# Kernel optimization log

Hardware: AMD Instinct MI355X
Metric: run time of the kernel (lower is better)

## Reference

```python
import jax, jax.numpy as jnp
import numpy as np

T, B, E, H = 2048, 2, 1024, 16
DH = E // H  # head_dim = 64


def setup_inputs() -> dict:
    key = jax.random.key(0)
    ks = jax.random.split(key, 5)
    query = jax.random.normal(ks[0], (T, B, E), dtype=jnp.float32)
    # self-attention: key/value are passed but unused by the module
    k_in = query
    v_in = query
    # xavier-ish scaled params
    in_proj_weight = jax.random.normal(ks[1], (3 * E, E), dtype=jnp.float32) * (E ** -0.5)
    in_proj_bias = jnp.zeros((3 * E,), dtype=jnp.float32)
    out_w = jax.random.normal(ks[2], (E, E), dtype=jnp.float32) * (E ** -0.5)
    out_b = jnp.zeros((E,), dtype=jnp.float32)
    return {"query": query, "key": k_in, "value": v_in,
            "in_proj_weight": in_proj_weight, "in_proj_bias": in_proj_bias,
            "out_w": out_w, "out_b": out_b}


def reference(query, key, value, in_proj_weight, in_proj_bias, out_w, out_b):
    # query: [T, B, E] (fairseq Time x Batch x Channel)
    t, b, e = query.shape
    scaling = DH ** -0.5
    # fused QKV projection: in_proj_weight [3E, E]
    qkv = jnp.einsum('tbe,fe->tbf', query, in_proj_weight) + in_proj_bias  # [T,B,3E]
    q, k, v = jnp.split(qkv, 3, axis=-1)
    q = q * scaling
    # split heads -> [T, B, H, DH]
    q = q.reshape(t, b, H, DH)
    k = k.reshape(t, b, H, DH)
    v = v.reshape(t, b, H, DH)
    # attention scores [B, H, T, T]
    scores = jnp.einsum('tbhd,sbhd->bhts', q, k)
    probs = jax.nn.softmax(scores, axis=-1)
    # weighted sum -> [T, B, H, DH] -> [T, B, E]
    attn = jnp.einsum('bhts,sbhd->tbhd', probs, v).reshape(t, b, e)
    # output projection (LinearSuper with sample dims == super dims)
    out = jnp.einsum('tbe,oe->tbo', attn, out_w) + out_b
    return out
```

## Files before the change

### kernel.cpp

```cpp
#include <hip/hip_runtime.h>
#include <hip/hip_bf16.h>
#include <stdint.h>
#include <math.h>

#define T_DIM 2048
#define B_DIM 2
#define E_DIM 1024
#define H_DIM 16
#define DH    64
#define MROWS (T_DIM * B_DIM)
#define QKVN  (3 * E_DIM)

typedef __attribute__((ext_vector_type(8))) __bf16 bf16x8;
typedef __attribute__((ext_vector_type(4))) float f32x4;
typedef __attribute__((ext_vector_type(4))) uint32_t u32x4;
typedef __attribute__((ext_vector_type(2))) uint32_t u32x2;

typedef __attribute__((address_space(1))) const uint32_t gu32;
typedef __attribute__((address_space(3))) uint32_t lu32;

#define GLL(gp, lp) __builtin_amdgcn_global_load_lds((gu32*)(gp), (lu32*)(lp), 16, 0, 0)

#define QSCALE 0.18033688011112042f

#if __has_builtin(__builtin_amdgcn_exp2f)
#define EXP2(x) __builtin_amdgcn_exp2f(x)
#else
#define EXP2(x) exp2f(x)
#endif

static __device__ __forceinline__ unsigned short f2bf(float f) {
    uint32_t u = __float_as_uint(f);
    u += 0x7FFFu + ((u >> 16) & 1u);
    return (unsigned short)(u >> 16);
}

__global__ void k_cvt3(const float* __restrict__ q,  const float* __restrict__ w,
                       const float* __restrict__ o,
                       unsigned short* __restrict__ qo, unsigned short* __restrict__ wo,
                       unsigned short* __restrict__ oo) {
    long i = (long)(blockIdx.x * 256 + threadIdx.x) * 8;
    const float* src; unsigned short* dst; long off;
    if (i < 4194304)      { src = q; dst = qo; off = i; }
    else if (i < 7340032) { src = w; dst = wo; off = i - 4194304; }
    else                  { src = o; dst = oo; off = i - 7340032; }
    float4 a = *(const float4*)(src + off);
    float4 b = *(const float4*)(src + off + 4);
    union { unsigned short s[8]; u32x4 v; } r;
    r.s[0] = f2bf(a.x); r.s[1] = f2bf(a.y); r.s[2] = f2bf(a.z); r.s[3] = f2bf(a.w);
    r.s[4] = f2bf(b.x); r.s[5] = f2bf(b.y); r.s[6] = f2bf(b.z); r.s[7] = f2bf(b.w);
    *(u32x4*)(dst + off) = r.v;
}

template <int STORE_BF16, int SCALE_Q>
__global__ __launch_bounds__(256) void k_gemm_bt(
    const unsigned short* __restrict__ A,
    const unsigned short* __restrict__ B,
    const float* __restrict__ bias,
    void* __restrict__ C,
    int M, int N, int K)
{
    __shared__ unsigned short As[128 * 64];
    __shared__ unsigned short Bs[128 * 64];
    const int tid = threadIdx.x;
    const int wid = tid >> 6, lane = tid & 63;
    const int m0 = blockIdx.y * 128, n0 = blockIdx.x * 128;

    const unsigned short* ag[4];
    const unsigned short* bg[4];
    unsigned lo[4];
#pragma unroll
    for (int j = 0; j < 4; ++j) {
        int o = (wid * 4 + j) * 1024 + lane * 16;
        int r = o >> 7;
        int c = (o >> 4) & 7;
        int cs = (c ^ (r & 7)) * 8;
        ag[j] = A + (long)(m0 + r) * K + cs;
        bg[j] = B + (long)(n0 + r) * K + cs;
        lo[j] = (unsigned)((wid * 4 + j) * 1024);
    }

    f32x4 acc[4][4] = {};
    const int wr = wid >> 1, wc = wid & 1;
    const int nk = K >> 6;

    for (int kt = 0; kt < nk; ++kt) {
#pragma unroll
        for (int j = 0; j < 4; ++j) {
            GLL(ag[j], (char*)As + lo[j]);
            GLL(bg[j], (char*)Bs + lo[j]);
            ag[j] += 64;
            bg[j] += 64;
        }
        __syncthreads();

        bf16x8 af[4][2], bfr[4][2];
#pragma unroll
        for (int i = 0; i < 4; ++i) {
            int ra = wr * 64 + i * 16 + (lane & 15);
            int rb = wc * 64 + i * 16 + (lane & 15);
#pragma unroll
            for (int kk = 0; kk < 2; ++kk) {
                int sa = ((kk * 4 + (lane >> 4)) ^ (ra & 7)) * 16;
                int sb = ((kk * 4 + (lane >> 4)) ^ (rb & 7)) * 16;
                af[i][kk]  = *(const bf16x8*)((char*)As + ra * 128 + sa);
                bfr[i][kk] = *(const bf16x8*)((char*)Bs + rb * 128 + sb);
            }
        }
#pragma unroll
        for (int kk = 0; kk < 2; ++kk)
#pragma unroll
            for (int mi = 0; mi < 4; ++mi)
#pragma unroll
                for (int ni = 0; ni < 4; ++ni)
                    acc[mi][ni] = __builtin_amdgcn_mfma_f32_16x16x32_bf16(
                        af[mi][kk], bfr[ni][kk], acc[mi][ni], 0, 0, 0);
        __syncthreads();
    }

#pragma unroll
    for (int mi = 0; mi < 4; ++mi)
#pragma unroll
        for (int ni = 0; ni < 4; ++ni) {
            int col = n0 + wc * 64 + ni * 16 + (lane & 15);
            float bv = bias[col];
            float scl = (SCALE_Q && col < 1024) ? QSCALE : 1.0f;
#pragma unroll
            for (int r = 0; r < 4; ++r) {
                int row = m0 + wr * 64 + mi * 16 + (lane >> 4) * 4 + r;
                float v = (acc[mi][ni][r] + bv) * scl;
                if (STORE_BF16)
                    ((unsigned short*)C)[(long)row * N + col] = f2bf(v);
                else
                    ((float*)C)[(long)row * N + col] = v;
            }
        }
}

__global__ __launch_bounds__(256) void k_transpose_v(
    const unsigned short* __restrict__ qkv, unsigned short* __restrict__ Vt)
{
    __shared__ unsigned short tile[64 * 64];
    const int bh = blockIdx.x >> 5, tt = blockIdx.x & 31;
    const int b = bh >> 4, h = bh & 15;
    const int tid = threadIdx.x;

    {
        int tr = tid >> 3;
        int s0 = tid & 7;
#pragma unroll
        for (int rr = 0; rr < 2; ++rr) {
            int t = tr + rr * 32;
            u32x4 v = *(const u32x4*)(qkv + ((long)(tt * 64 + t) * 2 + b) * 3072 + 2048 + h * 64 + s0 * 8);
            int slot = s0 ^ (t & 7) ^ ((t >> 3) & 7);
            *(u32x4*)((char*)tile + t * 128 + slot * 16) = v;
        }
    }
    __syncthreads();
    {
        int d = tid >> 3;
        int t8 = (tid & 7) * 8;
#pragma unroll
        for (int rr = 0; rr < 2; ++rr) {
            int dd = d + rr * 32;
            union { unsigned short s[8]; u32x4 v; } r;
#pragma unroll
            for (int i = 0; i < 8; ++i) {
                int pos = t8 + i;
                int t = (pos >> 2) + 16 * (pos & 3);
                int slot = (dd >> 3) ^ (t & 7) ^ ((t >> 3) & 7);
                r.s[i] = *(const unsigned short*)((char*)tile + t * 128 + slot * 16 + (dd & 7) * 2);
            }
            *(u32x4*)(Vt + ((long)bh * 64 + dd) * 2048 + tt * 64 + t8) = r.v;
        }
    }
}

__global__ __launch_bounds__(256, 2) void k_attn(
    const unsigned short* __restrict__ qkv,
    const unsigned short* __restrict__ Vt,
    unsigned short* __restrict__ attn)
{
    __shared__ unsigned short Ks[2 * 64 * 64];
    __shared__ unsigned short Vs[2 * 64 * 64];
    __shared__ unsigned short Ps[4 * 32 * 64];
    const int tid = threadIdx.x, wid = tid >> 6, lane = tid & 63;
    const int bh = blockIdx.x >> 4, tq = blockIdx.x & 15;
    const int b = bh >> 4, h = bh & 15;

    bf16x8 qf[2][2];
#pragma unroll
    for (int mi = 0; mi < 2; ++mi)
#pragma unroll
        for (int kk = 0; kk < 2; ++kk) {
            int t = tq * 128 + wid * 32 + mi * 16 + (lane & 15);
            qf[mi][kk] = *(const bf16x8*)(qkv + (long)(t * 2 + b) * 3072 + h * 64 + kk * 32 + (lane >> 4) * 8);
        }

    const unsigned short* kg[2];
    const unsigned short* vg[2];
    unsigned lo[2];
#pragma unroll
    for (int j = 0; j < 2; ++j) {
        int o = (wid * 2 + j) * 1024 + lane * 16;
        int r = o >> 7, c = (o >> 4) & 7;
        int cs = (c ^ (r & 7)) * 8;
        kg[j] = qkv + (long)(r * 2 + b) * 3072 + 1024 + h * 64 + cs;
        vg[j] = Vt + ((long)bh * 64 + r) * 2048 + cs;
        lo[j] = (unsigned)((wid * 2 + j) * 1024);
    }

    union { uint32_t u[4]; bf16x8 v; } onesu;
    onesu.u[0] = onesu.u[1] = onesu.u[2] = onesu.u[3] = 0x3F803F80u;
    const bf16x8 ones = onesu.v;

    f32x4 acc[2][4] = {};
    f32x4 suma[2] = {};

#pragma unroll
    for (int j = 0; j < 2; ++j) {
        GLL(kg[j], (char*)Ks + lo[j]);
        GLL(vg[j], (char*)Vs + lo[j]);
        kg[j] += 64 * 6144;
        vg[j] += 64;
    }

    for (int st = 0; st < 32; ++st) {
        const int cur = st & 1;
        if (st < 31) {
#pragma unroll
            for (int j = 0; j < 2; ++j) {
                GLL(kg[j], (char*)Ks + (cur ^ 1) * 8192 + lo[j]);
                GLL(vg[j], (char*)Vs + (cur ^ 1) * 8192 + lo[j]);
                kg[j] += 64 * 6144;
                vg[j] += 64;
            }
            asm volatile("s_waitcnt vmcnt(4)" ::: "memory");
        } else {
            asm volatile("s_waitcnt vmcnt(0)" ::: "memory");
        }
        __builtin_amdgcn_s_barrier();

        const char* kbase = (const char*)Ks + cur * 8192;
        const char* vbase = (const char*)Vs + cur * 8192;

        bf16x8 kf[4][2];
#pragma unroll
        for (int ni = 0; ni < 4; ++ni) {
            int row = ni * 16 + (lane & 15);
#pragma unroll
            for (int kk = 0; kk < 2; ++kk) {
                int sl = ((kk * 4 + (lane >> 4)) ^ (row & 7)) * 16;
                kf[ni][kk] = *(const bf16x8*)(kbase + row * 128 + sl);
            }
        }
        f32x4 sc[2][4] = {};
#pragma unroll
        for (int kk = 0; kk < 2; ++kk)
#pragma unroll
            for (int mi = 0; mi < 2; ++mi)
#pragma unroll
                for (int ni = 0; ni < 4; ++ni)
                    sc[mi][ni] = __builtin_amdgcn_mfma_f32_16x16x32_bf16(
                        qf[mi][kk], kf[ni][kk], sc[mi][ni], 0, 0, 0);

        const int c = lane & 15;
#pragma unroll
        for (int mi = 0; mi < 2; ++mi)
#pragma unroll
            for (int r = 0; r < 4; ++r) {
                float e0 = EXP2(sc[mi][0][r]);
                float e1 = EXP2(sc[mi][1][r]);
                float e2 = EXP2(sc[mi][2][r]);
                float e3 = EXP2(sc[mi][3][r]);
                int q = mi * 16 + (lane >> 4) * 4 + r;
                u32x2 w;
                w.x = (uint32_t)f2bf(e0) | ((uint32_t)f2bf(e1) << 16);
                w.y = (uint32_t)f2bf(e2) | ((uint32_t)f2bf(e3) << 16);
                int off = wid * 4096 + q * 128 + (((c >> 1) ^ (q & 7)) << 4) + (c & 1) * 8;
                *(u32x2*)((char*)Ps + off) = w;
            }

        bf16x8 pf[2][2], vf[4][2];
#pragma unroll
        for (int mi = 0; mi < 2; ++mi)
#pragma unroll
            for (int kk = 0; kk < 2; ++kk) {
                int q = mi * 16 + (lane & 15);
                int sl = ((kk * 4 + (lane >> 4)) ^ (q & 7)) * 16;
                pf[mi][kk] = *(const bf16x8*)((char*)Ps + wid * 4096 + q * 128 + sl);
            }
#pragma unroll
        for (int nd = 0; nd < 4; ++nd) {
            int row = nd * 16 + (lane & 15);
#pragma unroll
            for (int kk = 0; kk < 2; ++kk) {
                int sl = ((kk * 4 + (lane >> 4)) ^ (row & 7)) * 16;
                vf[nd][kk] = *(const bf16x8*)(vbase + row * 128 + sl);
            }
        }
#pragma unroll
        for (int kk = 0; kk < 2; ++kk)
#pragma unroll
            for (int mi = 0; mi < 2; ++mi) {
                suma[mi] = __builtin_amdgcn_mfma_f32_16x16x32_bf16(
                    pf[mi][kk], ones, suma[mi], 0, 0, 0);
#pragma unroll
                for (int nd = 0; nd < 4; ++nd)
                    acc[mi][nd] = __builtin_amdgcn_mfma_f32_16x16x32_bf16(
                        pf[mi][kk], vf[nd][kk], acc[mi][nd], 0, 0, 0);
            }
        __builtin_amdgcn_s_barrier();
    }

#pragma unroll
    for (int mi = 0; mi < 2; ++mi)
#pragma unroll
        for (int nd = 0; nd < 4; ++nd)
#pragma unroll
            for (int r = 0; r < 4; ++r) {
                int t = tq * 128 + wid * 32 + mi * 16 + (lane >> 4) * 4 + r;
                int e = h * 64 + nd * 16 + (lane & 15);
                attn[(long)(t * 2 + b) * 1024 + e] = f2bf(acc[mi][nd][r] / suma[mi][r]);
            }
}

extern "C" void kernel_launch(void* const* d_in, const int* in_sizes, int n_in,
                              void* d_out, int out_size, void* d_ws, size_t ws_size,
                              hipStream_t stream) {
    const float* query = (const float*)d_in[0];
    const float* ipw   = (const float*)d_in[3];
    const float* ipb   = (const float*)d_in[4];
    const float* ow    = (const float*)d_in[5];
    const float* ob    = (const float*)d_in[6];
    float* out = (float*)d_out;

    char* ws = (char*)d_ws;
    unsigned short* Xb   = (unsigned short*)(ws);
    unsigned short* Wb   = (unsigned short*)(ws + (8l << 20));
    unsigned short* OWb  = (unsigned short*)(ws + (14l << 20));
    unsigned short* qkvp = (unsigned short*)(ws + (16l << 20));
    unsigned short* Vtp  = (unsigned short*)(ws + (40l << 20));
    unsigned short* attn = (unsigned short*)(ws + (48l << 20));

    k_cvt3<<<4096, 256, 0, stream>>>(query, ipw, ow, Xb, Wb, OWb);

    k_gemm_bt<1, 1><<<dim3(QKVN / 128, MROWS / 128), 256, 0, stream>>>(
        Xb, Wb, ipb, qkvp, MROWS, QKVN, E_DIM);

    k_transpose_v<<<1024, 256, 0, stream>>>(qkvp, Vtp);

    k_attn<<<512, 256, 0, stream>>>(qkvp, Vtp, attn);

    k_gemm_bt<0, 0><<<dim3(E_DIM / 128, MROWS / 128), 256, 0, stream>>>(
        attn, OWb, ob, out, MROWS, E_DIM, E_DIM);
}
```

Measured before the change: 225.4 us.

## Software-pipeline attention loop so QK^T overlaps previous step's PV

```diff
diff --git a/kernel.cpp b/kernel.cpp
--- a/kernel.cpp
+++ b/kernel.cpp
@@ -183,7 +183,7 @@
 {
     __shared__ unsigned short Ks[2 * 64 * 64];
     __shared__ unsigned short Vs[2 * 64 * 64];
-    __shared__ unsigned short Ps[4 * 32 * 64];
+    __shared__ unsigned short Ps[2 * 4 * 32 * 64];
     const int tid = threadIdx.x, wid = tid >> 6, lane = tid & 63;
     const int bh = blockIdx.x >> 4, tq = blockIdx.x & 15;
     const int b = bh >> 4, h = bh & 15;
@@ -216,34 +216,26 @@
 
     f32x4 acc[2][4] = {};
     f32x4 suma[2] = {};
+    bf16x8 vf[4][2];
+
+    const int c = lane & 15;
 
 #pragma unroll
     for (int j = 0; j < 2; ++j) {
         GLL(kg[j], (char*)Ks + lo[j]);
         GLL(vg[j], (char*)Vs + lo[j]);
-        kg[j] += 64 * 6144;
-        vg[j] += 64;
-    }
-
-    for (int st = 0; st < 32; ++st) {
-        const int cur = st & 1;
-        if (st < 31) {
-#pragma unroll
-            for (int j = 0; j < 2; ++j) {
-                GLL(kg[j], (char*)Ks + (cur ^ 1) * 8192 + lo[j]);
-                GLL(vg[j], (char*)Vs + (cur ^ 1) * 8192 + lo[j]);
-                kg[j] += 64 * 6144;
-                vg[j] += 64;
-            }
-            asm volatile("s_waitcnt vmcnt(4)" ::: "memory");
-        } else {
-            asm volatile("s_waitcnt vmcnt(0)" ::: "memory");
-        }
-        __builtin_amdgcn_s_barrier();
-
-        const char* kbase = (const char*)Ks + cur * 8192;
-        const char* vbase = (const char*)Vs + cur * 8192;
-
+        kg[j] += 64 * 6144;  vg[j] += 64;
+    }
+#pragma unroll
+    for (int j = 0; j < 2; ++j) {
+        GLL(kg[j], (char*)Ks + 8192 + lo[j]);
+        GLL(vg[j], (char*)Vs + 8192 + lo[j]);
+        kg[j] += 64 * 6144;  vg[j] += 64;
+    }
+    asm volatile("s_waitcnt vmcnt(4)" ::: "memory");
+    __builtin_amdgcn_s_barrier();
+
+    {
         bf16x8 kf[4][2];
 #pragma unroll
         for (int ni = 0; ni < 4; ++ni) {
@@ -251,7 +243,7 @@
 #pragma unroll
             for (int kk = 0; kk < 2; ++kk) {
                 int sl = ((kk * 4 + (lane >> 4)) ^ (row & 7)) * 16;
-                kf[ni][kk] = *(const bf16x8*)(kbase + row * 128 + sl);
+                kf[ni][kk] = *(const bf16x8*)((char*)Ks + row * 128 + sl);
             }
         }
         f32x4 sc[2][4] = {};
@@ -263,8 +255,6 @@
                 for (int ni = 0; ni < 4; ++ni)
                     sc[mi][ni] = __builtin_amdgcn_mfma_f32_16x16x32_bf16(
                         qf[mi][kk], kf[ni][kk], sc[mi][ni], 0, 0, 0);
-
-        const int c = lane & 15;
 #pragma unroll
         for (int mi = 0; mi < 2; ++mi)
 #pragma unroll
@@ -280,25 +270,69 @@
                 int off = wid * 4096 + q * 128 + (((c >> 1) ^ (q & 7)) << 4) + (c & 1) * 8;
                 *(u32x2*)((char*)Ps + off) = w;
             }
-
-        bf16x8 pf[2][2], vf[4][2];
+#pragma unroll
+        for (int nd = 0; nd < 4; ++nd) {
+            int row = nd * 16 + (lane & 15);
+#pragma unroll
+            for (int kk = 0; kk < 2; ++kk) {
+                int sl = ((kk * 4 + (lane >> 4)) ^ (row & 7)) * 16;
+                vf[nd][kk] = *(const bf16x8*)((char*)Vs + row * 128 + sl);
+            }
+        }
+    }
+
+    for (int st = 1; st < 32; ++st) {
+        const int cur = st & 1;
+        asm volatile("s_waitcnt lgkmcnt(0)" ::: "memory");
+        __builtin_amdgcn_s_barrier();
+        __builtin_amdgcn_sched_barrier(0);
+        if (st < 31) {
+#pragma unroll
+            for (int j = 0; j < 2; ++j) {
+                GLL(kg[j], (char*)Ks + (cur ^ 1) * 8192 + lo[j]);
+                GLL(vg[j], (char*)Vs + (cur ^ 1) * 8192 + lo[j]);
+                kg[j] += 64 * 6144;  vg[j] += 64;
+            }
+            asm volatile("s_waitcnt vmcnt(4)" ::: "memory");
+        } else {
+            asm volatile("s_waitcnt vmcnt(0)" ::: "memory");
+        }
+        __builtin_amdgcn_s_barrier();
+
+        const char* kbase = (const char*)Ks + cur * 8192;
+        const char* vbase = (const char*)Vs + cur * 8192;
+        char* pw = (char*)Ps + cur * 16384 + wid * 4096;
+        const char* pr = (const char*)Ps + (cur ^ 1) * 16384 + wid * 4096;
+
+        bf16x8 kf[4][2];
+#pragma unroll
+        for (int ni = 0; ni < 4; ++ni) {
+            int row = ni * 16 + (lane & 15);
+#pragma unroll
+            for (int kk = 0; kk < 2; ++kk) {
+                int sl = ((kk * 4 + (lane >> 4)) ^ (row & 7)) * 16;
+                kf[ni][kk] = *(const bf16x8*)(kbase + row * 128 + sl);
+            }
+        }
+        f32x4 sc[2][4] = {};
+#pragma unroll
+        for (int kk = 0; kk < 2; ++kk)
+#pragma unroll
+            for (int mi = 0; mi < 2; ++mi)
+#pragma unroll
+                for (int ni = 0; ni < 4; ++ni)
+                    sc[mi][ni] = __builtin_amdgcn_mfma_f32_16x16x32_bf16(
+                        qf[mi][kk], kf[ni][kk], sc[mi][ni], 0, 0, 0);
+
+        bf16x8 pf[2][2];
 #pragma unroll
         for (int mi = 0; mi < 2; ++mi)
 #pragma unroll
             for (int kk = 0; kk < 2; ++kk) {
                 int q = mi * 16 + (lane & 15);
                 int sl = ((kk * 4 + (lane >> 4)) ^ (q & 7)) * 16;
-                pf[mi][kk] = *(const bf16x8*)((char*)Ps + wid * 4096 + q * 128 + sl);
-            }
-#pragma unroll
-        for (int nd = 0; nd < 4; ++nd) {
-            int row = nd * 16 + (lane & 15);
-#pragma unroll
-            for (int kk = 0; kk < 2; ++kk) {
-                int sl = ((kk * 4 + (lane >> 4)) ^ (row & 7)) * 16;
-                vf[nd][kk] = *(const bf16x8*)(vbase + row * 128 + sl);
-            }
-        }
+                pf[mi][kk] = *(const bf16x8*)(pr + q * 128 + sl);
+            }
 #pragma unroll
         for (int kk = 0; kk < 2; ++kk)
 #pragma unroll
@@ -310,7 +344,56 @@
                     acc[mi][nd] = __builtin_amdgcn_mfma_f32_16x16x32_bf16(
                         pf[mi][kk], vf[nd][kk], acc[mi][nd], 0, 0, 0);
             }
-        __builtin_amdgcn_s_barrier();
+
+#pragma unroll
+        for (int mi = 0; mi < 2; ++mi)
+#pragma unroll
+            for (int r = 0; r < 4; ++r) {
+                float e0 = EXP2(sc[mi][0][r]);
+                float e1 = EXP2(sc[mi][1][r]);
+                float e2 = EXP2(sc[mi][2][r]);
+                float e3 = EXP2(sc[mi][3][r]);
+                int q = mi * 16 + (lane >> 4) * 4 + r;
+                u32x2 w;
+                w.x = (uint32_t)f2bf(e0) | ((uint32_t)f2bf(e1) << 16);
+                w.y = (uint32_t)f2bf(e2) | ((uint32_t)f2bf(e3) << 16);
+                int off = q * 128 + (((c >> 1) ^ (q & 7)) << 4) + (c & 1) * 8;
+                *(u32x2*)(pw + off) = w;
+            }
+
+#pragma unroll
+        for (int nd = 0; nd < 4; ++nd) {
+            int row = nd * 16 + (lane & 15);
+#pragma unroll
+            for (int kk = 0; kk < 2; ++kk) {
+                int sl = ((kk * 4 + (lane >> 4)) ^ (row & 7)) * 16;
+                vf[nd][kk] = *(const bf16x8*)(vbase + row * 128 + sl);
+            }
+        }
+    }
+
+    {
+        const char* pr = (const char*)Ps + 16384 + wid * 4096;
+        bf16x8 pf[2][2];
+#pragma unroll
+        for (int mi = 0; mi < 2; ++mi)
+#pragma unroll
+            for (int kk = 0; kk < 2; ++kk) {
+                int q = mi * 16 + (lane & 15);
+                int sl = ((kk * 4 + (lane >> 4)) ^ (q & 7)) * 16;
+                pf[mi][kk] = *(const bf16x8*)(pr + q * 128 + sl);
+            }
+#pragma unroll
+        for (int kk = 0; kk < 2; ++kk)
+#pragma unroll
+            for (int mi = 0; mi < 2; ++mi) {
+                suma[mi] = __builtin_amdgcn_mfma_f32_16x16x32_bf16(
+                    pf[mi][kk], ones, suma[mi], 0, 0, 0);
+#pragma unroll
+                for (int nd = 0; nd < 4; ++nd)
+                    acc[mi][nd] = __builtin_amdgcn_mfma_f32_16x16x32_bf16(
+                        pf[mi][kk], vf[nd][kk], acc[mi][nd], 0, 0, 0);
+            }
     }
 
 #pragma unroll
```

Result: slower. 230.5 us (+2.2%).

## Keep softmax probabilities in registers by transposing MFMA operands and permuting V

Applied to the files above, without the earlier changes.

```diff
diff --git a/kernel.cpp b/kernel.cpp
--- a/kernel.cpp
+++ b/kernel.cpp
@@ -167,7 +167,7 @@
 #pragma unroll
             for (int i = 0; i < 8; ++i) {
                 int pos = t8 + i;
-                int t = (pos >> 2) + 16 * (pos & 3);
+                int t = 4 * ((pos >> 3) & 3) + (pos & 3) + 16 * (2 * (pos >> 5) + ((pos >> 2) & 1));
                 int slot = (dd >> 3) ^ (t & 7) ^ ((t >> 3) & 7);
                 r.s[i] = *(const unsigned short*)((char*)tile + t * 128 + slot * 16 + (dd & 7) * 2);
             }
@@ -183,7 +183,6 @@
 {
     __shared__ unsigned short Ks[2 * 64 * 64];
     __shared__ unsigned short Vs[2 * 64 * 64];
-    __shared__ unsigned short Ps[4 * 32 * 64];
     const int tid = threadIdx.x, wid = tid >> 6, lane = tid & 63;
     const int bh = blockIdx.x >> 4, tq = blockIdx.x & 15;
     const int b = bh >> 4, h = bh & 15;
@@ -210,12 +209,8 @@
         lo[j] = (unsigned)((wid * 2 + j) * 1024);
     }
 
-    union { uint32_t u[4]; bf16x8 v; } onesu;
-    onesu.u[0] = onesu.u[1] = onesu.u[2] = onesu.u[3] = 0x3F803F80u;
-    const bf16x8 ones = onesu.v;
-
     f32x4 acc[2][4] = {};
-    f32x4 suma[2] = {};
+    float suma[2] = {0.f, 0.f};
 
 #pragma unroll
     for (int j = 0; j < 2; ++j) {
@@ -262,67 +257,73 @@
 #pragma unroll
                 for (int ni = 0; ni < 4; ++ni)
                     sc[mi][ni] = __builtin_amdgcn_mfma_f32_16x16x32_bf16(
-                        qf[mi][kk], kf[ni][kk], sc[mi][ni], 0, 0, 0);
-
-        const int c = lane & 15;
-#pragma unroll
-        for (int mi = 0; mi < 2; ++mi)
-#pragma unroll
-            for (int r = 0; r < 4; ++r) {
-                float e0 = EXP2(sc[mi][0][r]);
-                float e1 = EXP2(sc[mi][1][r]);
-                float e2 = EXP2(sc[mi][2][r]);
-                float e3 = EXP2(sc[mi][3][r]);
-                int q = mi * 16 + (lane >> 4) * 4 + r;
-                u32x2 w;
-                w.x = (uint32_t)f2bf(e0) | ((uint32_t)f2bf(e1) << 16);
-                w.y = (uint32_t)f2bf(e2) | ((uint32_t)f2bf(e3) << 16);
-                int off = wid * 4096 + q * 128 + (((c >> 1) ^ (q & 7)) << 4) + (c & 1) * 8;
-                *(u32x2*)((char*)Ps + off) = w;
-            }
-
-        bf16x8 pf[2][2], vf[4][2];
-#pragma unroll
-        for (int mi = 0; mi < 2; ++mi)
-#pragma unroll
-            for (int kk = 0; kk < 2; ++kk) {
-                int q = mi * 16 + (lane & 15);
-                int sl = ((kk * 4 + (lane >> 4)) ^ (q & 7)) * 16;
-                pf[mi][kk] = *(const bf16x8*)((char*)Ps + wid * 4096 + q * 128 + sl);
-            }
+                        kf[ni][kk], qf[mi][kk], sc[mi][ni], 0, 0, 0);
+
+        bf16x8 pfrag[2][2];
+#pragma unroll
+        for (int mi = 0; mi < 2; ++mi) {
+            float ex[4][4];
+            float part = 0.f;
+#pragma unroll
+            for (int ni = 0; ni < 4; ++ni)
+#pragma unroll
+                for (int r = 0; r < 4; ++r) {
+                    float e = EXP2(sc[mi][ni][r]);
+                    ex[ni][r] = e;
+                    part += e;
+                }
+            suma[mi] += part;
+#pragma unroll
+            for (int a = 0; a < 2; ++a) {
+                union { uint32_t u[4]; bf16x8 v; } pk;
+                pk.u[0] = (uint32_t)f2bf(ex[2 * a][0])     | ((uint32_t)f2bf(ex[2 * a][1]) << 16);
+                pk.u[1] = (uint32_t)f2bf(ex[2 * a][2])     | ((uint32_t)f2bf(ex[2 * a][3]) << 16);
+                pk.u[2] = (uint32_t)f2bf(ex[2 * a + 1][0]) | ((uint32_t)f2bf(ex[2 * a + 1][1]) << 16);
+                pk.u[3] = (uint32_t)f2bf(ex[2 * a + 1][2]) | ((uint32_t)f2bf(ex[2 * a + 1][3]) << 16);
+                pfrag[mi][a] = pk.v;
+            }
+        }
+
+        bf16x8 vf[4][2];
 #pragma unroll
         for (int nd = 0; nd < 4; ++nd) {
             int row = nd * 16 + (lane & 15);
 #pragma unroll
-            for (int kk = 0; kk < 2; ++kk) {
-                int sl = ((kk * 4 + (lane >> 4)) ^ (row & 7)) * 16;
-                vf[nd][kk] = *(const bf16x8*)(vbase + row * 128 + sl);
-            }
-        }
-#pragma unroll
-        for (int kk = 0; kk < 2; ++kk)
-#pragma unroll
-            for (int mi = 0; mi < 2; ++mi) {
-                suma[mi] = __builtin_amdgcn_mfma_f32_16x16x32_bf16(
-                    pf[mi][kk], ones, suma[mi], 0, 0, 0);
+            for (int a = 0; a < 2; ++a) {
+                int sl = ((a * 4 + (lane >> 4)) ^ (row & 7)) * 16;
+                vf[nd][a] = *(const bf16x8*)(vbase + row * 128 + sl);
+            }
+        }
+#pragma unroll
+        for (int a = 0; a < 2; ++a)
+#pragma unroll
+            for (int mi = 0; mi < 2; ++mi)
 #pragma unroll
                 for (int nd = 0; nd < 4; ++nd)
                     acc[mi][nd] = __builtin_amdgcn_mfma_f32_16x16x32_bf16(
-                        pf[mi][kk], vf[nd][kk], acc[mi][nd], 0, 0, 0);
-            }
+                        vf[nd][a], pfrag[mi][a], acc[mi][nd], 0, 0, 0);
         __builtin_amdgcn_s_barrier();
     }
 
 #pragma unroll
-    for (int mi = 0; mi < 2; ++mi)
-#pragma unroll
-        for (int nd = 0; nd < 4; ++nd)
-#pragma unroll
-            for (int r = 0; r < 4; ++r) {
-                int t = tq * 128 + wid * 32 + mi * 16 + (lane >> 4) * 4 + r;
-                int e = h * 64 + nd * 16 + (lane & 15);
-                attn[(long)(t * 2 + b) * 1024 + e] = f2bf(acc[mi][nd][r] / suma[mi][r]);
-            }
+    for (int mi = 0; mi < 2; ++mi) {
+        suma[mi] += __shfl_xor(suma[mi], 16, 64);
+        suma[mi] += __shfl_xor(suma[mi], 32, 64);
+    }
+
+#pragma unroll
+    for (int mi = 0; mi < 2; ++mi) {
+        float inv = 1.0f / suma[mi];
+        int t = tq * 128 + wid * 32 + mi * 16 + (lane & 15);
+#pragma unroll
+        for (int nd = 0; nd < 4; ++nd) {
+            int e = h * 64 + nd * 16 + (lane >> 4) * 4;
+            u32x2 w;
+            w.x = (uint32_t)f2bf(acc[mi][nd][0] * inv) | ((uint32_t)f2bf(acc[mi][nd][1] * inv) << 16);
+            w.y = (uint32_t)f2bf(acc[mi][nd][2] * inv) | ((uint32_t)f2bf(acc[mi][nd][3] * inv) << 16);
+            *(u32x2*)(attn + (long)(t * 2 + b) * 1024 + e) = w;
+        }
+    }
 }
 
 extern "C" void kernel_launch(void* const* d_in, const int* in_sizes, int n_in,
```

After: 223.2 us. About the same (-1.0%).
